# Kernel optimization log

Hardware: AMD Instinct MI355X
Metric: run time of the kernel (lower is better)

The kernel has to match this reference:

```python
import jax, jax.numpy as jnp
import numpy as np

N = 1024        # batch of tokens (module is per-token; we vmap via batched einsums)
IN = 1024       # in_features
H = 16          # num_heads
D = 64          # head_dim
BD = 512        # binary_dim
M = 8192        # num memories
OUT = H * D     # out_features
TEMP = 0.01
EPS = 1e-5


def setup_inputs() -> dict:
    key = jax.random.key(0)
    ks = jax.random.split(key, 8)
    return {
        "x": jax.random.normal(ks[0], (N, IN), jnp.float32),
        "Wq": jax.random.normal(ks[1], (OUT, IN), jnp.float32) / np.sqrt(IN).astype(np.float32),
        "bq_bias": jax.random.normal(ks[2], (OUT,), jnp.float32) * 0.01,
        "bin_proj": jax.random.normal(ks[3], (H, BD, D), jnp.float32),
        "bin_inv": jax.random.normal(ks[4], (H, D, BD), jnp.float32) / np.float32(BD),
        # binary memory codes in {-1, +1}
        "weight_matrix": jnp.sign(jax.random.normal(ks[5], (H, M, BD), jnp.float32)),
        "ln_w": jnp.ones((OUT,), jnp.float32),
        "ln_b": jnp.zeros((OUT,), jnp.float32),
    }


def reference(x, Wq, bq_bias, bin_proj, bin_inv, weight_matrix, ln_w, ln_b):
    # query projection: [N, OUT] -> [N, H, D], L2-normalize per head
    q = (x @ Wq.T + bq_bias).reshape(N, H, D)
    q = q / jnp.linalg.norm(q, axis=-1, keepdims=True)
    # sign-encode into binary space: [N, H, BD]
    code = jnp.sign(jnp.einsum('nhd,hbd->nhb', q, bin_proj))
    # cosine-transformed Hamming-similarity scores: [N, H, M]
    sim = jnp.einsum('nhb,hmb->nhm', code, weight_matrix) / np.float32(BD)
    scores = jnp.cos((np.float32(np.pi) / 2) * (1.0 - sim))
    attn = jax.nn.softmax(scores / np.float32(TEMP), axis=-1)
    # readout from binary memories, project back to real space
    out = jnp.einsum('nhm,hmb->nhb', attn, weight_matrix)
    out = jnp.einsum('nhb,hdb->nhd', out, bin_inv)
    out = out / jnp.linalg.norm(out, axis=-1, keepdims=True)
    out = out.reshape(N, OUT)
    # LayerNorm over out_features
    mu = jnp.mean(out, axis=-1, keepdims=True)
    var = jnp.var(out, axis=-1, keepdims=True)
    return (out - mu) / jnp.sqrt(var + np.float32(EPS)) * ln_w + ln_b
```

## Files before the change

kernel.cpp:

```cpp
#include <hip/hip_runtime.h>
#include <hip/hip_fp16.h>

#define NTOK 1024
#define INF  1024
#define NH   16
#define DH   64
#define BDIM 512
#define NMEM 8192
#define OUTF 1024
#define NWRD 16

typedef _Float16 f16x8 __attribute__((ext_vector_type(8)));
typedef float    f32x4 __attribute__((ext_vector_type(4)));
typedef int      i32x4 __attribute__((ext_vector_type(4)));

#define GLOAD16(G, L) __builtin_amdgcn_global_load_lds( \
    (const __attribute__((address_space(1))) unsigned int*)(G), \
    (__attribute__((address_space(3))) unsigned int*)(L), 16, 0, 0)

__device__ inline float score2(float s) {
  return 144.2695040889f * __sinf(s * 0.0030679615757712823f);
}

__global__ __launch_bounds__(256) void k_qgemm(const float* __restrict__ x,
    const float* __restrict__ Wq, const float* __restrict__ bq, float* __restrict__ q) {
  __shared__ float As[64][17];
  __shared__ float Bs[64][17];
  const int tx = threadIdx.x & 15, ty = threadIdx.x >> 4;
  const int n0 = blockIdx.y * 64, o0 = blockIdx.x * 64;
  const int r = threadIdx.x >> 2, c4 = (threadIdx.x & 3) * 4;
  float acc[4][4] = {};
  for (int k0 = 0; k0 < INF; k0 += 16) {
    float4 av = *(const float4*)&x[(size_t)(n0 + r) * INF + k0 + c4];
    float4 bv = *(const float4*)&Wq[(size_t)(o0 + r) * INF + k0 + c4];
    __syncthreads();
    As[r][c4+0] = av.x; As[r][c4+1] = av.y; As[r][c4+2] = av.z; As[r][c4+3] = av.w;
    Bs[r][c4+0] = bv.x; Bs[r][c4+1] = bv.y; Bs[r][c4+2] = bv.z; Bs[r][c4+3] = bv.w;
    __syncthreads();
    #pragma unroll
    for (int kk = 0; kk < 16; ++kk) {
      float a[4], b[4];
      #pragma unroll
      for (int i = 0; i < 4; ++i) a[i] = As[ty*4+i][kk];
      #pragma unroll
      for (int j = 0; j < 4; ++j) b[j] = Bs[tx*4+j][kk];
      #pragma unroll
      for (int i = 0; i < 4; ++i)
        #pragma unroll
        for (int j = 0; j < 4; ++j) acc[i][j] += a[i] * b[j];
    }
  }
  #pragma unroll
  for (int i = 0; i < 4; ++i) {
    const int row = n0 + ty*4 + i;
    #pragma unroll
    for (int j = 0; j < 4; ++j) {
      const int col = o0 + tx*4 + j;
      q[(size_t)row * OUTF + col] = acc[i][j] + bq[col];
    }
  }
}

__global__ __launch_bounds__(256) void k_code(const float* __restrict__ q,
    const float* __restrict__ bp, signed char* __restrict__ code_i8) {
  const int h = blockIdx.y, n0 = blockIdx.x * 16;
  __shared__ float ql[16][68];
  const int t = threadIdx.x;
  {
    const int r = t >> 4, c = (t & 15) * 4;
    float4 v = *(const float4*)&q[(size_t)(n0 + r) * OUTF + h * 64 + c];
    ql[r][c] = v.x; ql[r][c+1] = v.y; ql[r][c+2] = v.z; ql[r][c+3] = v.w;
  }
  __syncthreads();
  #pragma unroll
  for (int bb = 0; bb < 512; bb += 256) {
    const int b = bb + t;
    float bpv[64];
    const float4* src = (const float4*)&bp[((size_t)h * BDIM + b) * 64];
    #pragma unroll
    for (int j = 0; j < 16; ++j) {
      float4 v = src[j];
      bpv[j*4] = v.x; bpv[j*4+1] = v.y; bpv[j*4+2] = v.z; bpv[j*4+3] = v.w;
    }
    for (int n = 0; n < 16; ++n) {
      float dot = 0.f;
      #pragma unroll
      for (int d = 0; d < 64; ++d) dot += bpv[d] * ql[n][d];
      code_i8[((size_t)h * NTOK + n0 + n) * BDIM + b] = dot > 0.f ? 1 : -1;
    }
  }
}

__global__ __launch_bounds__(256) void k_packw(const float* __restrict__ w,
    unsigned* __restrict__ wp, signed char* __restrict__ w_i8) {
  const int row  = blockIdx.x * 4 + (threadIdx.x >> 6);
  const int lane = threadIdx.x & 63;
  const float* src = w + (size_t)row * BDIM;
  unsigned my = 0;
  #pragma unroll
  for (int kk = 0; kk < 8; ++kk) {
    float v = src[kk * 64 + lane];
    const int c = kk * 4 + (lane >> 4);
    const int p = (c & ~7) | ((c & 7) ^ (row & 7));
    w_i8[(size_t)row * BDIM + p * 16 + (lane & 15)] = v > 0.f ? 1 : -1;
    unsigned long long m = __ballot(v > 0.f);
    if ((lane >> 1) == kk) my = (lane & 1) ? (unsigned)(m >> 32) : (unsigned)m;
  }
  if (lane < 16) wp[(size_t)row * NWRD + lane] = my;
}

__global__ __launch_bounds__(256) void k_binT(const float* __restrict__ binv,
                                              float* __restrict__ bT) {
  const int h = blockIdx.y, b0 = blockIdx.x * 64;
  __shared__ float tl[64][65];
  const int t = threadIdx.x;
  #pragma unroll
  for (int i = 0; i < 4; ++i) {
    int fi = t + 256 * i;
    int d = fi >> 4, b = (fi & 15) * 4;
    float4 v = *(const float4*)&binv[((size_t)h * DH + d) * BDIM + b0 + b];
    tl[d][b] = v.x; tl[d][b+1] = v.y; tl[d][b+2] = v.z; tl[d][b+3] = v.w;
  }
  __syncthreads();
  #pragma unroll
  for (int i = 0; i < 4; ++i) {
    int fo = t + 256 * i;
    int bb = fo >> 4, dd = (fo & 15) * 4;
    float4 v = { tl[dd][bb], tl[dd+1][bb], tl[dd+2][bb], tl[dd+3][bb] };
    *(float4*)&bT[((size_t)h * BDIM + b0 + bb) * DH + dd] = v;
  }
}

__global__ __launch_bounds__(256) void k_wt(const unsigned* __restrict__ wp,
    unsigned short* __restrict__ wt, int h0) {
  const int hg = blockIdx.z, h = h0 + hg;
  const int b0 = blockIdx.y * 64, m0 = blockIdx.x * 256;
  __shared__ unsigned bits[256][2];
  const int t = threadIdx.x;
  const unsigned* src = wp + (size_t)(h * NMEM + m0 + t) * NWRD + (b0 >> 5);
  bits[t][0] = src[0]; bits[t][1] = src[1];
  __syncthreads();
  const int b = t >> 2, ms = (t & 3) * 64;
  const int wd = b >> 5, sh = b & 31;
  const int bx7 = b & 7;
  unsigned short* dst = wt + ((size_t)hg * BDIM + b0 + b) * NMEM + m0 + ms;
  #pragma unroll
  for (int g = 0; g < 8; ++g) {
    const int pg = g ^ bx7;
    const int j = ms + g * 8;
    ushort4 v0, v1;
    v0.x = ((bits[j+0][wd] >> sh) & 1) ? 0x3C00 : 0xBC00;
    v0.y = ((bits[j+1][wd] >> sh) & 1) ? 0x3C00 : 0xBC00;
    v0.z = ((bits[j+2][wd] >> sh) & 1) ? 0x3C00 : 0xBC00;
    v0.w = ((bits[j+3][wd] >> sh) & 1) ? 0x3C00 : 0xBC00;
    v1.x = ((bits[j+4][wd] >> sh) & 1) ? 0x3C00 : 0xBC00;
    v1.y = ((bits[j+5][wd] >> sh) & 1) ? 0x3C00 : 0xBC00;
    v1.z = ((bits[j+6][wd] >> sh) & 1) ? 0x3C00 : 0xBC00;
    v1.w = ((bits[j+7][wd] >> sh) & 1) ? 0x3C00 : 0xBC00;
    *(ushort4*)&dst[pg * 8]     = v0;
    *(ushort4*)&dst[pg * 8 + 4] = v1;
  }
}

__global__ __launch_bounds__(512, 2) void k_sim(const signed char* __restrict__ code_i8,
    const signed char* __restrict__ w_i8, short* __restrict__ simb,
    int h0, int gmask, int gshift) {
  const int bid = (int)blockIdx.x;
  const int hg = bid & gmask, h = h0 + hg;
  const int n0 = (bid >> gshift) * 32;
  const int t = threadIdx.x, lane = t & 63, wid = t >> 6;
  __shared__ __align__(16) signed char Bls[128 * 512];
  __shared__ float sct[513];
  __shared__ int smaxl[32];
  if (t < 32) smaxl[t] = -(1 << 30);
  for (int p = t; p < 513; p += 512)
    sct[p] = score2(2.f * (float)p - 512.f);
  const int rg = wid >> 2, mg = wid & 3;
  i32x4 afrag[8];
  #pragma unroll
  for (int kk = 0; kk < 8; ++kk)
    afrag[kk] = *(const i32x4*)(code_i8 +
        ((size_t)h * NTOK + n0 + rg * 16 + (lane & 15)) * BDIM +
        kk * 64 + (lane >> 4) * 16);
  const signed char* wb = w_i8 + (size_t)h * NMEM * BDIM + (size_t)t * 16;
  signed char* const d0 = &Bls[wid * 1024];
  int vmax[4] = {-(1 << 30), -(1 << 30), -(1 << 30), -(1 << 30)};
  short* srow = simb + ((size_t)hg * NTOK + n0) * NMEM;
  for (int tile = 0; tile < 64; ++tile) {
    const signed char* s = wb + (size_t)tile * 128 * BDIM;
    __syncthreads();
    #pragma unroll
    for (int seg = 0; seg < 8; ++seg)
      GLOAD16(s + seg * 8192, d0 + seg * 8192);
    __syncthreads();
    #pragma unroll
    for (int msub = 0; msub < 2; ++msub) {
      const signed char* bls = &Bls[(mg * 32 + msub * 16 + (lane & 15)) * 512];
      i32x4 acc = {};
      #pragma unroll
      for (int kk = 0; kk < 8; ++kk) {
        const int c = kk * 4 + (lane >> 4);
        const int p = (c & ~7) | ((c & 7) ^ (lane & 7));
        i32x4 b = *(const i32x4*)(bls + p * 16);
        acc = __builtin_amdgcn_mfma_i32_16x16x64_i8(afrag[kk], b, acc, 0, 0, 0);
      }
      const int m0 = tile * 128 + mg * 32 + msub * 16 + (lane & 15);
      #pragma unroll
      for (int j = 0; j < 4; ++j) {
        const int r0 = rg * 16 + (lane >> 4) * 4 + j;
        srow[(size_t)r0 * NMEM + m0] = (short)acc[j];
        vmax[j] = max(vmax[j], acc[j]);
      }
    }
  }
  #pragma unroll
  for (int j = 0; j < 4; ++j) {
    int v = vmax[j];
    #pragma unroll
    for (int s = 1; s < 16; s <<= 1) v = max(v, __shfl_xor(v, s));
    if ((lane & 15) == 0)
      atomicMax(&smaxl[rg * 16 + (lane >> 4) * 4 + j], v);
  }
  __syncthreads();
  unsigned short* arow = (unsigned short*)srow;
  for (int it = 0; it < 8; ++it) {
    const int gw = it * 512 + t;
    const int row = gw >> 7, win = gw & 127;
    const float sm2 = sct[(smaxl[row] + 512) >> 1];
    const short* sp = srow + (size_t)row * NMEM + win * 64;
    uint4 sv[8];
    #pragma unroll
    for (int c = 0; c < 8; ++c) sv[c] = *(const uint4*)(sp + c * 8);
    const int rx = row & 7;
    unsigned short* dp = arow + (size_t)row * NMEM + win * 64;
    #pragma unroll
    for (int c = 0; c < 8; ++c) {
      unsigned ov[4];
      #pragma unroll
      for (int k = 0; k < 4; ++k) {
        const unsigned w2 = (&sv[c].x)[k];
        const int lo = (int)(short)(w2 & 0xffffu);
        const int hi = (int)(short)(w2 >> 16);
        float p0 = exp2f(sct[(lo + 512) >> 1] - sm2);
        float p1 = exp2f(sct[(hi + 512) >> 1] - sm2);
        ov[k] = (unsigned)__half_as_ushort(__float2half(p0))
              | ((unsigned)__half_as_ushort(__float2half(p1)) << 16);
      }
      *(uint4*)(dp + (c ^ rx) * 8) = make_uint4(ov[0], ov[1], ov[2], ov[3]);
    }
  }
}

__global__ __launch_bounds__(512, 2) void k_stageF(const unsigned short* __restrict__ attn,
    const unsigned short* __restrict__ wt, float* __restrict__ o1t,
    int gmask, int gshift) {
  __shared__ __align__(16) _Float16 Al[128][64];
  __shared__ __align__(16) _Float16 Bl[128][64];
  const int wg = (int)blockIdx.x;
  const int hg = wg & gmask;
  const int rest = wg >> gshift;
  const int nt = rest & 7, bt = rest >> 3;
  const int n0 = nt * 128, b0 = bt * 128;
  const int t = threadIdx.x;
  const int lane = t & 63, wid = t >> 6;
  const int wm = wid >> 2, wn = wid & 3;
  f32x4 acc[4][2];
  #pragma unroll
  for (int i = 0; i < 4; ++i)
    #pragma unroll
    for (int j = 0; j < 2; ++j) acc[i][j] = (f32x4){0.f, 0.f, 0.f, 0.f};

  const unsigned short* ag = attn + ((size_t)hg * NTOK + n0 + 16*wid + (lane >> 3)) * NMEM + (lane & 7) * 8;
  const unsigned short* bg = wt   + ((size_t)hg * BDIM + b0 + 16*wid + (lane >> 3)) * NMEM + (lane & 7) * 8;
  _Float16* al0 = &Al[16 * wid][0];
  _Float16* bl0 = &Bl[16 * wid][0];

  for (int k0 = 0; k0 < NMEM; k0 += 64) {
    __syncthreads();
    GLOAD16(ag + k0,            al0);
    GLOAD16(ag + k0 + 8 * NMEM, al0 + 8 * 64);
    GLOAD16(bg + k0,            bl0);
    GLOAD16(bg + k0 + 8 * NMEM, bl0 + 8 * 64);
    __syncthreads();
    #pragma unroll
    for (int kk = 0; kk < 64; kk += 32) {
      const int phys = (((kk >> 3) + (lane >> 4)) ^ (lane & 7)) * 8;
      f16x8 af[4], bf[2];
      #pragma unroll
      for (int fm = 0; fm < 4; ++fm)
        af[fm] = *(const f16x8*)&Al[wm*64 + fm*16 + (lane & 15)][phys];
      #pragma unroll
      for (int fn = 0; fn < 2; ++fn)
        bf[fn] = *(const f16x8*)&Bl[wn*32 + fn*16 + (lane & 15)][phys];
      #pragma unroll
      for (int fm = 0; fm < 4; ++fm)
        #pragma unroll
        for (int fn = 0; fn < 2; ++fn)
          acc[fm][fn] = __builtin_amdgcn_mfma_f32_16x16x32_f16(af[fm], bf[fn], acc[fm][fn], 0, 0, 0);
    }
  }
  #pragma unroll
  for (int fm = 0; fm < 4; ++fm) {
    const int rowb = n0 + wm*64 + fm*16 + (lane >> 4) * 4;
    #pragma unroll
    for (int fn = 0; fn < 2; ++fn) {
      const int col = b0 + wn*32 + fn*16 + (lane & 15);
      *(f32x4*)&o1t[((size_t)hg * BDIM + col) * NTOK + rowb] = acc[fm][fn];
    }
  }
}

__global__ __launch_bounds__(256) void k_proj(const float* __restrict__ o1t,
    const float* __restrict__ bT, float* __restrict__ o2, int h0) {
  const int hg = blockIdx.y, h = h0 + hg;
  const int n0 = blockIdx.x * 64;
  __shared__ float bl[128][68];
  __shared__ float ol[128][68];
  __shared__ float outl[64][68];
  __shared__ float nrm[64];
  const int t = threadIdx.x;
  const int tx = t & 15, ty = t >> 4;
  float acc[4][4] = {};
  for (int c = 0; c < 4; ++c) {
    const int bb0 = c * 128;
    __syncthreads();
    #pragma unroll
    for (int i = 0; i < 8; ++i) {
      int fi = t + 256 * i;
      int rr = fi >> 4, cc = (fi & 15) * 4;
      *(float4*)&bl[rr][cc] = *(const float4*)&bT[((size_t)h * BDIM + bb0 + rr) * DH + cc];
      *(float4*)&ol[rr][cc] = *(const float4*)&o1t[((size_t)hg * BDIM + bb0 + rr) * NTOK + n0 + cc];
    }
    __syncthreads();
    for (int bb = 0; bb < 128; ++bb) {
      float4 bd = *(const float4*)&bl[bb][tx * 4];
      float4 on = *(const float4*)&ol[bb][ty * 4];
      float ai[4] = {on.x, on.y, on.z, on.w};
      float bj[4] = {bd.x, bd.y, bd.z, bd.w};
      #pragma unroll
      for (int i = 0; i < 4; ++i)
        #pragma unroll
        for (int j = 0; j < 4; ++j) acc[i][j] += ai[i] * bj[j];
    }
  }
  __syncthreads();
  #pragma unroll
  for (int i = 0; i < 4; ++i)
    #pragma unroll
    for (int j = 0; j < 4; ++j) outl[ty*4 + i][tx*4 + j] = acc[i][j];
  __syncthreads();
  if (t < 64) {
    float s = 0.f;
    #pragma unroll
    for (int d = 0; d < 64; ++d) { float v = outl[t][d]; s += v * v; }
    nrm[t] = 1.f / sqrtf(s);
  }
  __syncthreads();
  {
    const int n = t >> 2, dg = (t & 3) * 16;
    #pragma unroll
    for (int j = 0; j < 16; ++j)
      o2[(size_t)(n0 + n) * OUTF + h * 64 + dg + j] = outl[n][dg + j] * nrm[n];
  }
}

__global__ __launch_bounds__(256) void k_ln(const float* __restrict__ o2,
    const float* __restrict__ lnw, const float* __restrict__ lnb, float* __restrict__ out) {
  const int n = blockIdx.x, t = threadIdx.x;
  __shared__ float red[4];
  float4 v = *(const float4*)&o2[(size_t)n * OUTF + t * 4];
  float s = v.x + v.y + v.z + v.w;
  const int lane = t & 63, wid = t >> 6;
  #pragma unroll
  for (int off = 32; off; off >>= 1) s += __shfl_down(s, off);
  if (lane == 0) red[wid] = s;
  __syncthreads();
  const float mu = (red[0] + red[1] + red[2] + red[3]) * (1.f / 1024.f);
  float4 d = {v.x - mu, v.y - mu, v.z - mu, v.w - mu};
  float s2 = d.x*d.x + d.y*d.y + d.z*d.z + d.w*d.w;
  #pragma unroll
  for (int off = 32; off; off >>= 1) s2 += __shfl_down(s2, off);
  __syncthreads();
  if (lane == 0) red[wid] = s2;
  __syncthreads();
  const float var = (red[0] + red[1] + red[2] + red[3]) * (1.f / 1024.f);
  const float inv = 1.f / sqrtf(var + 1e-5f);
  float4 w = *(const float4*)&lnw[t * 4];
  float4 b = *(const float4*)&lnb[t * 4];
  float4 o = { d.x*inv*w.x + b.x, d.y*inv*w.y + b.y,
               d.z*inv*w.z + b.z, d.w*inv*w.w + b.w };
  *(float4*)&out[(size_t)n * OUTF + t * 4] = o;
}

extern "C" void kernel_launch(void* const* d_in, const int* in_sizes, int n_in,
                              void* d_out, int out_size, void* d_ws, size_t ws_size,
                              hipStream_t stream) {
  (void)in_sizes; (void)n_in; (void)out_size;
  const float* x    = (const float*)d_in[0];
  const float* Wq   = (const float*)d_in[1];
  const float* bq   = (const float*)d_in[2];
  const float* bp   = (const float*)d_in[3];
  const float* binv = (const float*)d_in[4];
  const float* wm   = (const float*)d_in[5];
  const float* lnw  = (const float*)d_in[6];
  const float* lnb  = (const float*)d_in[7];
  float* outp = (float*)d_out;

  char* ws = (char*)d_ws;
  size_t off = 0;
  auto carve = [&](size_t bytes) -> char* {
    char* p = ws + off;
    off += (bytes + 255) & ~(size_t)255;
    return p;
  };
  float*       q       = (float*)      carve((size_t)NTOK * OUTF * 4);
  signed char* code_i8 = (signed char*)carve((size_t)NH * NTOK * BDIM);
  unsigned*    wpk     = (unsigned*)   carve((size_t)NH * NMEM * NWRD * 4);
  signed char* w_i8    = (signed char*)carve((size_t)NH * NMEM * BDIM);
  float*       bT      = (float*)      carve((size_t)NH * BDIM * DH * 4);
  float*       o2      = (float*)      carve((size_t)NTOK * OUTF * 4);
  const size_t fixed = off;
  const size_t per = ((size_t)BDIM * NMEM * 2 + 256)
                   + ((size_t)NTOK * NMEM * 2 + 256)
                   + ((size_t)BDIM * NTOK * 4 + 256);
  int G = 16;
  while (G > 1 && fixed + (size_t)G * per > ws_size) G >>= 1;
  unsigned short* wt   = (unsigned short*)carve((size_t)G * BDIM * NMEM * 2);
  short*          simb = (short*)         carve((size_t)G * NTOK * NMEM * 2);
  float*          o1t  = (float*)         carve((size_t)G * BDIM * NTOK * 4);
  const int gshift = __builtin_ctz(G);

  k_qgemm<<<dim3(16, 16), 256, 0, stream>>>(x, Wq, bq, q);
  k_code <<<dim3(64, 16), 256, 0, stream>>>(q, bp, code_i8);
  k_packw<<<dim3(NH * NMEM / 4), 256, 0, stream>>>(wm, wpk, w_i8);
  k_binT <<<dim3(8, 16), 256, 0, stream>>>(binv, bT);
  for (int h0 = 0; h0 < NH; h0 += G) {
    k_wt    <<<dim3(32, 8, G), 256, 0, stream>>>(wpk, wt, h0);
    k_sim   <<<dim3(32 * G),   512, 0, stream>>>(code_i8, w_i8, simb, h0, G - 1, gshift);
    k_stageF<<<dim3(32 * G),   512, 0, stream>>>((const unsigned short*)simb, wt, o1t, G - 1, gshift);
    k_proj  <<<dim3(16, G),    256, 0, stream>>>(o1t, bT, o2, h0);
  }
  k_ln<<<dim3(NTOK), 256, 0, stream>>>(o2, lnw, lnb, outp);
}
```

Before: 758.8 us.

## Recompute similarity scores in a second pass instead of spilling int16 sims to HBM

k_sim now runs the int8 MFMA similarity GEMM twice. The first pass only finds the row max. The second pass recomputes the scores, applies the exp directly, and stages the fp16 probabilities in LDS before writing them out with coalesced swizzled stores. This removes the write-then-read round trip of the int16 similarity buffer through global memory, at the cost of doubling the MFMA work and the memory-tile loads in k_sim. The score lookup table is replaced by computing __sinf directly per element.

```diff
diff --git a/kernel.cpp b/kernel.cpp
--- a/kernel.cpp
+++ b/kernel.cpp
@@ -163,18 +163,16 @@
 }
 
 __global__ __launch_bounds__(512, 2) void k_sim(const signed char* __restrict__ code_i8,
-    const signed char* __restrict__ w_i8, short* __restrict__ simb,
+    const signed char* __restrict__ w_i8, unsigned short* __restrict__ attn,
     int h0, int gmask, int gshift) {
   const int bid = (int)blockIdx.x;
   const int hg = bid & gmask, h = h0 + hg;
   const int n0 = (bid >> gshift) * 32;
   const int t = threadIdx.x, lane = t & 63, wid = t >> 6;
   __shared__ __align__(16) signed char Bls[128 * 512];
-  __shared__ float sct[513];
+  __shared__ __align__(16) _Float16 Pls[32][136];
   __shared__ int smaxl[32];
   if (t < 32) smaxl[t] = -(1 << 30);
-  for (int p = t; p < 513; p += 512)
-    sct[p] = score2(2.f * (float)p - 512.f);
   const int rg = wid >> 2, mg = wid & 3;
   i32x4 afrag[8];
   #pragma unroll
@@ -185,7 +183,6 @@
   const signed char* wb = w_i8 + (size_t)h * NMEM * BDIM + (size_t)t * 16;
   signed char* const d0 = &Bls[wid * 1024];
   int vmax[4] = {-(1 << 30), -(1 << 30), -(1 << 30), -(1 << 30)};
-  short* srow = simb + ((size_t)hg * NTOK + n0) * NMEM;
   for (int tile = 0; tile < 64; ++tile) {
     const signed char* s = wb + (size_t)tile * 128 * BDIM;
     __syncthreads();
@@ -204,13 +201,8 @@
         i32x4 b = *(const i32x4*)(bls + p * 16);
         acc = __builtin_amdgcn_mfma_i32_16x16x64_i8(afrag[kk], b, acc, 0, 0, 0);
       }
-      const int m0 = tile * 128 + mg * 32 + msub * 16 + (lane & 15);
-      #pragma unroll
-      for (int j = 0; j < 4; ++j) {
-        const int r0 = rg * 16 + (lane >> 4) * 4 + j;
-        srow[(size_t)r0 * NMEM + m0] = (short)acc[j];
-        vmax[j] = max(vmax[j], acc[j]);
-      }
+      #pragma unroll
+      for (int j = 0; j < 4; ++j) vmax[j] = max(vmax[j], acc[j]);
     }
   }
   #pragma unroll
@@ -222,32 +214,48 @@
       atomicMax(&smaxl[rg * 16 + (lane >> 4) * 4 + j], v);
   }
   __syncthreads();
-  unsigned short* arow = (unsigned short*)srow;
-  for (int it = 0; it < 8; ++it) {
-    const int gw = it * 512 + t;
-    const int row = gw >> 7, win = gw & 127;
-    const float sm2 = sct[(smaxl[row] + 512) >> 1];
-    const short* sp = srow + (size_t)row * NMEM + win * 64;
-    uint4 sv[8];
-    #pragma unroll
-    for (int c = 0; c < 8; ++c) sv[c] = *(const uint4*)(sp + c * 8);
-    const int rx = row & 7;
-    unsigned short* dp = arow + (size_t)row * NMEM + win * 64;
-    #pragma unroll
-    for (int c = 0; c < 8; ++c) {
-      unsigned ov[4];
-      #pragma unroll
-      for (int k = 0; k < 4; ++k) {
-        const unsigned w2 = (&sv[c].x)[k];
-        const int lo = (int)(short)(w2 & 0xffffu);
-        const int hi = (int)(short)(w2 >> 16);
-        float p0 = exp2f(sct[(lo + 512) >> 1] - sm2);
-        float p1 = exp2f(sct[(hi + 512) >> 1] - sm2);
-        ov[k] = (unsigned)__half_as_ushort(__float2half(p0))
-              | ((unsigned)__half_as_ushort(__float2half(p1)) << 16);
+  float sm[4];
+  #pragma unroll
+  for (int j = 0; j < 4; ++j)
+    sm[j] = score2((float)smaxl[rg * 16 + (lane >> 4) * 4 + j]);
+  const int srow = t >> 4, sg = t & 15;
+  unsigned short* const sdst = attn + ((size_t)hg * NTOK + n0 + srow) * NMEM;
+  const int spc = ((sg & 7) ^ (srow & 7)) * 8 + (sg >> 3) * 64;
+  for (int tile = 0; tile < 64; ++tile) {
+    const signed char* s = wb + (size_t)tile * 128 * BDIM;
+    __syncthreads();
+    #pragma unroll
+    for (int seg = 0; seg < 8; ++seg)
+      GLOAD16(s + seg * 8192, d0 + seg * 8192);
+    if (tile > 0) {
+      f16x8 pv = *(const f16x8*)&Pls[srow][sg * 8];
+      *(f16x8*)(sdst + (size_t)(tile - 1) * 128 + spc) = pv;
+    }
+    __syncthreads();
+    #pragma unroll
+    for (int msub = 0; msub < 2; ++msub) {
+      const signed char* bls = &Bls[(mg * 32 + msub * 16 + (lane & 15)) * 512];
+      i32x4 acc = {};
+      #pragma unroll
+      for (int kk = 0; kk < 8; ++kk) {
+        const int c = kk * 4 + (lane >> 4);
+        const int p = (c & ~7) | ((c & 7) ^ (lane & 7));
+        i32x4 b = *(const i32x4*)(bls + p * 16);
+        acc = __builtin_amdgcn_mfma_i32_16x16x64_i8(afrag[kk], b, acc, 0, 0, 0);
       }
-      *(uint4*)(dp + (c ^ rx) * 8) = make_uint4(ov[0], ov[1], ov[2], ov[3]);
-    }
+      const int col = mg * 32 + msub * 16 + (lane & 15);
+      #pragma unroll
+      for (int j = 0; j < 4; ++j) {
+        const int r0 = rg * 16 + (lane >> 4) * 4 + j;
+        float pr = exp2f(score2((float)acc[j]) - sm[j]);
+        Pls[r0][col] = (_Float16)pr;
+      }
+    }
+  }
+  __syncthreads();
+  {
+    f16x8 pv = *(const f16x8*)&Pls[srow][sg * 8];
+    *(f16x8*)(sdst + (size_t)63 * 128 + spc) = pv;
   }
 }
 
@@ -426,7 +434,7 @@
   int G = 16;
   while (G > 1 && fixed + (size_t)G * per > ws_size) G >>= 1;
   unsigned short* wt   = (unsigned short*)carve((size_t)G * BDIM * NMEM * 2);
-  short*          simb = (short*)         carve((size_t)G * NTOK * NMEM * 2);
+  unsigned short* attn = (unsigned short*)carve((size_t)G * NTOK * NMEM * 2);
   float*          o1t  = (float*)         carve((size_t)G * BDIM * NTOK * 4);
   const int gshift = __builtin_ctz(G);
 
@@ -436,8 +444,8 @@
   k_binT <<<dim3(8, 16), 256, 0, stream>>>(binv, bT);
   for (int h0 = 0; h0 < NH; h0 += G) {
     k_wt    <<<dim3(32, 8, G), 256, 0, stream>>>(wpk, wt, h0);
-    k_sim   <<<dim3(32 * G),   512, 0, stream>>>(code_i8, w_i8, simb, h0, G - 1, gshift);
-    k_stageF<<<dim3(32 * G),   512, 0, stream>>>((const unsigned short*)simb, wt, o1t, G - 1, gshift);
+    k_sim   <<<dim3(32 * G),   512, 0, stream>>>(code_i8, w_i8, attn, h0, G - 1, gshift);
+    k_stageF<<<dim3(32 * G),   512, 0, stream>>>(attn, wt, o1t, G - 1, gshift);
     k_proj  <<<dim3(16, G),    256, 0, stream>>>(o1t, bT, o2, h0);
   }
   k_ln<<<dim3(NTOK), 256, 0, stream>>>(o2, lnw, lnb, outp);
```

Result: faster. 738.3 us (-2.7%).
